# Optimization experiments

Measured on AMD Instinct MI355X. Metric: run time of the kernel, lower is better.

The kernel has to match this reference:

```python
import jax, jax.numpy as jnp
import numpy as np

B, T, D = 2, 2048, 2048
H, KV, HD = 16, 4, 128
EPS = 1e-6


def _rmsnorm(x, scale):
    # flax.linen.RMSNorm over last axis: x / sqrt(mean(x^2) + eps) * scale
    var = jnp.mean(jnp.square(x), axis=-1, keepdims=True)
    return x * jax.lax.rsqrt(var + EPS) * scale


def _rope(x, cos, sin):
    # x: [b, t, h, d]; cos/sin: [t, d]
    x_rot = jnp.stack([-x[..., 1::2], x[..., 0::2]], axis=-1)
    x_rot = x_rot.reshape(*x_rot.shape[:-2], -1)
    return x * cos[None, :, None, :] + x_rot * sin[None, :, None, :]


def setup_inputs() -> dict:
    key = jax.random.key(0)
    ks = jax.random.split(key, 5)
    x = jax.random.normal(ks[0], (B, T, D), jnp.float32)
    Wq = jax.random.normal(ks[1], (D, H * HD), jnp.float32) / np.sqrt(D)
    Wk = jax.random.normal(ks[2], (D, KV * HD), jnp.float32) / np.sqrt(D)
    Wv = jax.random.normal(ks[3], (D, KV * HD), jnp.float32) / np.sqrt(D)
    Wo = jax.random.normal(ks[4], (H * HD, D), jnp.float32) / np.sqrt(H * HD)
    q_scale = jnp.ones((HD,), jnp.float32)
    k_scale = jnp.ones((HD,), jnp.float32)
    # standard RoPE tables, interleaved-pair convention
    pos = jnp.arange(T, dtype=jnp.float32)
    inv_freq = 1.0 / (10000.0 ** (jnp.arange(0, HD, 2, dtype=jnp.float32) / HD))
    freqs = pos[:, None] * inv_freq[None, :]  # [T, HD/2]
    cos = jnp.repeat(jnp.cos(freqs), 2, axis=-1)  # [T, HD]
    sin = jnp.repeat(jnp.sin(freqs), 2, axis=-1)
    mask = jnp.tril(jnp.ones((T, T), bool))[None, None]  # causal [1,1,T,T]
    return {"x": x, "Wq": Wq, "Wk": Wk, "Wv": Wv, "Wo": Wo,
            "q_scale": q_scale, "k_scale": k_scale,
            "cos": cos, "sin": sin, "mask": mask}


def reference(x, Wq, Wk, Wv, Wo, q_scale, k_scale, cos, sin, mask):
    num_groups = H // KV
    q = (x @ Wq).reshape(B, T, H, HD)
    k = (x @ Wk).reshape(B, T, KV, HD)
    v = (x @ Wv).reshape(B, T, KV, HD)
    q = _rmsnorm(q, q_scale)
    k = _rmsnorm(k, k_scale)
    q = _rope(q, cos, sin)
    k = _rope(k, cos, sin)
    k = jnp.repeat(k, num_groups, axis=2)  # [b, t, H, d]
    v = jnp.repeat(v, num_groups, axis=2)
    scores = jnp.einsum('bqhd,bkhd->bhqk', q, k) / jnp.sqrt(jnp.float32(HD))
    scores = jnp.where(mask, scores, jnp.finfo(scores.dtype).min)
    attn = jax.nn.softmax(scores, axis=-1)
    out = jnp.einsum('bhqk,bkhd->bqhd', attn, v)
    out = out.reshape(B, T, H * HD)
    return out @ Wo
```

## Files before the change

kernel.cpp:

```cpp
#include <hip/hip_runtime.h>
#include <hip/hip_bf16.h>

#define B_   2
#define T_   2048
#define D_   2048
#define H_   16
#define KV_  4
#define HD_  128
#define BT_  (B_*T_)
#define QKVP 3072
#define KOFF 2048
#define VOFF 2560
static constexpr float EPS_ = 1e-6f;

typedef unsigned short u16;
typedef __attribute__((ext_vector_type(8))) short short8;
typedef __attribute__((ext_vector_type(4))) float f32x4;
typedef __attribute__((ext_vector_type(4))) unsigned short u16x4;

__device__ __forceinline__ u16 f2bf(float f){
    unsigned u = __float_as_uint(f);
    u += 0x7FFF + ((u >> 16) & 1);
    return (u16)(u >> 16);
}
__device__ __forceinline__ float bf2f(u16 u){
    return __uint_as_float((unsigned)u << 16);
}

__device__ __forceinline__ void async_copy16(const void* g, void* l) {
    __builtin_amdgcn_global_load_lds(
        (const __attribute__((address_space(1))) unsigned int*)g,
        (__attribute__((address_space(3))) unsigned int*)l, 16, 0, 0);
}

__global__ __launch_bounds__(256) void cvt_f32_bf16_kernel(
    const float* __restrict__ in, u16* __restrict__ out, int n)
{
    const int i = (blockIdx.x*256 + threadIdx.x)*4;
    if (i < n) {
        float4 v = *(const float4*)&in[i];
        u16x4 w = { f2bf(v.x), f2bf(v.y), f2bf(v.z), f2bf(v.w) };
        *(u16x4*)&out[i] = w;
    }
}

__global__ __launch_bounds__(256) void transpose_cvt_kernel(
    const float* __restrict__ in, u16* __restrict__ out, int R, int C)
{
    __shared__ u16 tile[64][65];
    const int r0 = blockIdx.y*64, c0 = blockIdx.x*64;
    const int tr = threadIdx.x >> 4;
    const int tc = (threadIdx.x & 15) * 4;
    #pragma unroll
    for (int i = 0; i < 4; i++) {
        const int r = tr + i*16;
        float4 v = *(const float4*)&in[(size_t)(r0 + r)*C + c0 + tc];
        tile[tc+0][r] = f2bf(v.x);
        tile[tc+1][r] = f2bf(v.y);
        tile[tc+2][r] = f2bf(v.z);
        tile[tc+3][r] = f2bf(v.w);
    }
    __syncthreads();
    #pragma unroll
    for (int i = 0; i < 4; i++) {
        const int c = tr + i*16;
        u16x4 w = { tile[c][tc+0], tile[c][tc+1], tile[c][tc+2], tile[c][tc+3] };
        *(u16x4*)&out[(size_t)(c0 + c)*R + r0 + tc] = w;
    }
}

__global__ __launch_bounds__(256) void transpose_v_kernel(
    const u16* __restrict__ qkv, u16* __restrict__ vt)
{
    __shared__ u16 tile[64][65];
    const int t0 = blockIdx.x*64;
    const int d0 = blockIdx.y*64;
    const int bk = blockIdx.z;
    const int tr = threadIdx.x >> 4;
    const int tc = (threadIdx.x & 15) * 4;
    #pragma unroll
    for (int i = 0; i < 4; i++) {
        const int t = t0 + tr + i*16;
        u16x4 v = *(const u16x4*)&qkv[(size_t)((bk>>2)*T_ + t)*QKVP + VOFF
                                      + (bk&3)*HD_ + d0 + tc];
        tile[tc+0][tr+i*16] = v[0];
        tile[tc+1][tr+i*16] = v[1];
        tile[tc+2][tr+i*16] = v[2];
        tile[tc+3][tr+i*16] = v[3];
    }
    __syncthreads();
    #pragma unroll
    for (int i = 0; i < 4; i++) {
        const int d = tr + i*16;
        u16x4 w = { tile[d][tc+0], tile[d][tc+1], tile[d][tc+2], tile[d][tc+3] };
        *(u16x4*)&vt[((size_t)bk*HD_ + d0 + d)*T_ + t0 + tc] = w;
    }
}

#define GBM 128
#define GBN 128
#define GBK 32

template<bool OUT_BF16>
__global__ __launch_bounds__(256) void gemm_mfma_kernel(
    const u16* __restrict__ A, const u16* __restrict__ Bt,
    void* __restrict__ C, int N, int K, int lda, int ldb, int ldc)
{
    __shared__ __align__(16) u16 As[GBM][GBK];
    __shared__ __align__(16) u16 Bs[GBN][GBK];
    const int tid  = threadIdx.x;
    const int lane = tid & 63;
    const int wave = tid >> 6;
    const int l15  = lane & 15;
    const int quad = lane >> 4;
    const int wr   = (wave >> 1) * 64;
    const int wc   = (wave & 1) * 64;
    const size_t row0 = (size_t)blockIdx.y * GBM;
    const size_t col0 = (size_t)blockIdx.x * GBN;

    f32x4 acc[4][4];
    #pragma unroll
    for (int i = 0; i < 4; i++)
        #pragma unroll
        for (int j = 0; j < 4; j++)
            acc[i][j] = (f32x4){0.f,0.f,0.f,0.f};

    for (int k0 = 0; k0 < K; k0 += GBK) {
        #pragma unroll
        for (int c = 0; c < 2; c++) {
            const int e = (c*256 + tid) * 8;
            const int r = e >> 5, cc = e & 31;
            async_copy16(A  + (row0 + r)*lda + k0 + cc, &As[r][cc]);
            async_copy16(Bt + (col0 + r)*ldb + k0 + cc, &Bs[r][cc]);
        }
        __syncthreads();

        short8 af[4], bf[4];
        #pragma unroll
        for (int i = 0; i < 4; i++)
            af[i] = *(const short8*)&As[wr + i*16 + l15][quad*8];
        #pragma unroll
        for (int j = 0; j < 4; j++)
            bf[j] = *(const short8*)&Bs[wc + j*16 + l15][quad*8];
        #pragma unroll
        for (int i = 0; i < 4; i++)
            #pragma unroll
            for (int j = 0; j < 4; j++)
                acc[i][j] = __builtin_amdgcn_mfma_f32_16x16x32_bf16(
                    af[i], bf[j], acc[i][j], 0, 0, 0);
        __syncthreads();
    }

    #pragma unroll
    for (int i = 0; i < 4; i++)
        #pragma unroll
        for (int r = 0; r < 4; r++) {
            const size_t row = row0 + wr + i*16 + quad*4 + r;
            #pragma unroll
            for (int j = 0; j < 4; j++) {
                const size_t col = col0 + wc + j*16 + l15;
                if (OUT_BF16) ((u16*)C)[row*ldc + col] = f2bf(acc[i][j][r]);
                else          ((float*)C)[row*ldc + col] = acc[i][j][r];
            }
        }
}

__global__ __launch_bounds__(256) void rmsnorm_rope_kernel(
    u16* __restrict__ qk, const float* __restrict__ scale,
    const float* __restrict__ cosT, const float* __restrict__ sinT,
    int heads_per_token, int head_off, float post_scale)
{
    const int wid   = blockIdx.x*4 + (threadIdx.x >> 6);
    const int lane  = threadIdx.x & 63;
    const int token = wid / heads_per_token;
    const int hidx  = wid % heads_per_token;
    const int t     = token & (T_ - 1);
    u16* p = qk + (size_t)token*QKVP + head_off + hidx*HD_ + lane*2;

    const unsigned u = *(const unsigned*)p;
    const float x0 = bf2f((u16)(u & 0xffff));
    const float x1 = bf2f((u16)(u >> 16));
    float ss = x0*x0 + x1*x1;
    #pragma unroll
    for (int off = 32; off > 0; off >>= 1) ss += __shfl_xor(ss, off);
    const float rms = rsqrtf(ss * (1.0f/HD_) + EPS_);

    const float2 sc = *(const float2*)&scale[lane*2];
    const float2 cs = *(const float2*)&cosT[(size_t)t*HD_ + lane*2];
    const float2 sn = *(const float2*)&sinT[(size_t)t*HD_ + lane*2];
    const float n0 = x0 * rms * sc.x;
    const float n1 = x1 * rms * sc.y;
    const float r0 = (n0*cs.x - n1*sn.x) * post_scale;
    const float r1 = (n1*cs.y + n0*sn.y) * post_scale;
    *(unsigned*)p = (unsigned)f2bf(r0) | ((unsigned)f2bf(r1) << 16);
}

#define BQ  64
#define BKV 64

__global__ __launch_bounds__(256, 2) void attn_mfma7_kernel(
    const u16* __restrict__ qkv, const u16* __restrict__ Vtg)
{
    __shared__ __align__(16) u16 Ks[2][16][BKV][8];
    __shared__ __align__(16) u16 Vt[2][8][HD_][8];
    __shared__ __align__(16) u16 Pb[64][88];
    __shared__ float SumX[2][64];

    const int pr   = blockIdx.x;
    const int h    = blockIdx.y;
    const int b    = blockIdx.z;
    const int kvh  = h >> 2;
    const int tid  = threadIdx.x;
    const int lane = tid & 63;
    const int wave = tid >> 6;
    const int rh   = wave >> 1;
    const int kh   = wave & 1;
    const int l15  = lane & 15;
    const int quad = lane >> 4;
    const int NT   = T_ / BQ;

    for (int phase = 0; phase < 2; phase++) {
        const int qt = phase ? pr : (NT - 1 - pr);
        const int q0 = qt * BQ;

        short8 qf[2][4];
        #pragma unroll
        for (int rf = 0; rf < 2; rf++) {
            const u16* qbase = qkv + (size_t)(b*T_ + q0 + rh*32 + rf*16 + l15)*QKVP + h*HD_;
            #pragma unroll
            for (int kt = 0; kt < 4; kt++)
                qf[rf][kt] = *(const short8*)(qbase + kt*32 + quad*8);
        }

        float lsum[2][4];
        #pragma unroll
        for (int rf = 0; rf < 2; rf++)
            #pragma unroll
            for (int r = 0; r < 4; r++) lsum[rf][r] = 0.f;
        f32x4 oacc[2][4];
        #pragma unroll
        for (int rf = 0; rf < 2; rf++)
            #pragma unroll
            for (int cv = 0; cv < 4; cv++) oacc[rf][cv] = (f32x4){0.f,0.f,0.f,0.f};

        const int ntiles = qt + 1;

        #pragma unroll
        for (int it = 0; it < 4; it++) {
            const int n   = it*256 + tid;
            const int cc  = n >> 6;
            const int key = n & 63;
            async_copy16(qkv + (size_t)(b*T_ + key)*QKVP + KOFF + kvh*HD_ + cc*8,
                         &Ks[0][cc][key][0]);
        }
        #pragma unroll
        for (int it = 0; it < 4; it++) {
            const int n  = it*256 + tid;
            const int cc = n >> 7;
            const int d  = n & 127;
            async_copy16(Vtg + ((size_t)(b*KV_ + kvh)*HD_ + d)*T_ + cc*8,
                         &Vt[0][cc][d][0]);
        }
        __syncthreads();

        int cur = 0;
        for (int t = 0; t < ntiles; t++) {
            if (t + 1 < ntiles) {
                const int k0n = (t + 1) * BKV;
                #pragma unroll
                for (int it = 0; it < 4; it++) {
                    const int n   = it*256 + tid;
                    const int cc  = n >> 6;
                    const int key = n & 63;
                    async_copy16(qkv + (size_t)(b*T_ + k0n + key)*QKVP + KOFF + kvh*HD_ + cc*8,
                                 &Ks[cur^1][cc][key][0]);
                }
                #pragma unroll
                for (int it = 0; it < 4; it++) {
                    const int n  = it*256 + tid;
                    const int cc = n >> 7;
                    const int d  = n & 127;
                    async_copy16(Vtg + ((size_t)(b*KV_ + kvh)*HD_ + d)*T_ + k0n + cc*8,
                                 &Vt[cur^1][cc][d][0]);
                }
            }

            const int k0 = t * BKV;

            f32x4 s[2][2];
            #pragma unroll
            for (int rf = 0; rf < 2; rf++)
                #pragma unroll
                for (int cj = 0; cj < 2; cj++) s[rf][cj] = (f32x4){0.f,0.f,0.f,0.f};
            __builtin_amdgcn_s_setprio(1);
            #pragma unroll
            for (int kt = 0; kt < 4; kt++) {
                #pragma unroll
                for (int cj = 0; cj < 2; cj++) {
                    short8 kf = *(const short8*)&Ks[cur][kt*4 + quad][kh*32 + cj*16 + l15][0];
                    #pragma unroll
                    for (int rf = 0; rf < 2; rf++)
                        s[rf][cj] = __builtin_amdgcn_mfma_f32_16x16x32_bf16(
                            qf[rf][kt], kf, s[rf][cj], 0, 0, 0);
                }
            }
            __builtin_amdgcn_s_setprio(0);

            if (t == ntiles - 1) {
                #pragma unroll
                for (int rf = 0; rf < 2; rf++) {
                    const int qrow0 = q0 + rh*32 + rf*16 + quad*4;
                    #pragma unroll
                    for (int r = 0; r < 4; r++)
                        #pragma unroll
                        for (int cj = 0; cj < 2; cj++) {
                            const int key = k0 + kh*32 + cj*16 + l15;
                            if (key > qrow0 + r) s[rf][cj][r] = -1e30f;
                        }
                }
            }
            #pragma unroll
            for (int rf = 0; rf < 2; rf++)
                #pragma unroll
                for (int r = 0; r < 4; r++)
                    #pragma unroll
                    for (int cj = 0; cj < 2; cj++) {
                        const float p = __expf(s[rf][cj][r]);
                        s[rf][cj][r] = p;
                        lsum[rf][r] += p;
                        Pb[rh*32 + rf*16 + quad*4 + r][kh*32 + cj*16 + l15] = f2bf(p);
                    }

            asm volatile("s_waitcnt lgkmcnt(0)" ::: "memory");
            __builtin_amdgcn_s_barrier();

            __builtin_amdgcn_s_setprio(1);
            #pragma unroll
            for (int kt2 = 0; kt2 < 2; kt2++) {
                short8 pa[2];
                #pragma unroll
                for (int rf = 0; rf < 2; rf++)
                    pa[rf] = *(const short8*)&Pb[rh*32 + rf*16 + l15][kt2*32 + quad*8];
                #pragma unroll
                for (int cv = 0; cv < 4; cv++) {
                    short8 vf = *(const short8*)&Vt[cur][kt2*4 + quad][kh*64 + cv*16 + l15][0];
                    #pragma unroll
                    for (int rf = 0; rf < 2; rf++)
                        oacc[rf][cv] = __builtin_amdgcn_mfma_f32_16x16x32_bf16(
                            pa[rf], vf, oacc[rf][cv], 0, 0, 0);
                }
            }
            __builtin_amdgcn_s_setprio(0);

            __syncthreads();
            cur ^= 1;
        }

        #pragma unroll
        for (int rf = 0; rf < 2; rf++)
            #pragma unroll
            for (int r = 0; r < 4; r++) {
                float tot = lsum[rf][r];
                #pragma unroll
                for (int off = 1; off < 16; off <<= 1)
                    tot += __shfl_xor(tot, off, 16);
                if (l15 == 0) SumX[kh][rh*32 + rf*16 + quad*4 + r] = tot;
            }
        __syncthreads();
        #pragma unroll
        for (int rf = 0; rf < 2; rf++)
            #pragma unroll
            for (int r = 0; r < 4; r++) {
                const int rIdx = rh*32 + rf*16 + quad*4 + r;
                const float linv = 1.0f / (SumX[0][rIdx] + SumX[1][rIdx]);
                u16* orow = (u16*)qkv + (size_t)(b*T_ + q0 + rIdx)*QKVP
                            + h*HD_ + kh*64 + l15;
                #pragma unroll
                for (int cv = 0; cv < 4; cv++)
                    orow[cv*16] = f2bf(oacc[rf][cv][r] * linv);
            }
        __syncthreads();
    }
}

extern "C" void kernel_launch(void* const* d_in, const int* in_sizes, int n_in,
                              void* d_out, int out_size, void* d_ws, size_t ws_size,
                              hipStream_t stream)
{
    const float* x    = (const float*)d_in[0];
    const float* Wq   = (const float*)d_in[1];
    const float* Wk   = (const float*)d_in[2];
    const float* Wv   = (const float*)d_in[3];
    const float* Wo   = (const float*)d_in[4];
    const float* qsc  = (const float*)d_in[5];
    const float* ksc  = (const float*)d_in[6];
    const float* cosT = (const float*)d_in[7];
    const float* sinT = (const float*)d_in[8];
    float* out = (float*)d_out;

    u16* xb     = (u16*)d_ws;
    u16* Wqkvt  = xb    + (size_t)BT_*D_;
    u16* Wot    = Wqkvt + (size_t)QKVP*D_;
    u16* qkv    = Wot   + (size_t)D_*(H_*HD_);
    u16* vtg    = qkv   + (size_t)BT_*QKVP;

    cvt_f32_bf16_kernel<<<(BT_*D_)/1024, 256, 0, stream>>>(x, xb, BT_*D_);
    transpose_cvt_kernel<<<dim3((H_*HD_)/64,  D_/64), 256, 0, stream>>>(
        Wq, Wqkvt, D_, H_*HD_);
    transpose_cvt_kernel<<<dim3((KV_*HD_)/64, D_/64), 256, 0, stream>>>(
        Wk, Wqkvt + (size_t)KOFF*D_, D_, KV_*HD_);
    transpose_cvt_kernel<<<dim3((KV_*HD_)/64, D_/64), 256, 0, stream>>>(
        Wv, Wqkvt + (size_t)VOFF*D_, D_, KV_*HD_);
    transpose_cvt_kernel<<<dim3(D_/64, (H_*HD_)/64),  256, 0, stream>>>(
        Wo, Wot, H_*HD_, D_);

    gemm_mfma_kernel<true><<<dim3(QKVP/GBN, BT_/GBM), 256, 0, stream>>>(
        xb, Wqkvt, qkv, QKVP, D_, D_, D_, QKVP);

    rmsnorm_rope_kernel<<<(BT_*H_)/4,  256, 0, stream>>>(
        qkv, qsc, cosT, sinT, H_, 0, 0.08838834764831845f);
    rmsnorm_rope_kernel<<<(BT_*KV_)/4, 256, 0, stream>>>(
        qkv, ksc, cosT, sinT, KV_, KOFF, 1.0f);

    transpose_v_kernel<<<dim3(T_/64, HD_/64, B_*KV_), 256, 0, stream>>>(qkv, vtg);

    attn_mfma7_kernel<<<dim3(T_/BQ/2, H_, B_), 256, 0, stream>>>(qkv, vtg);

    gemm_mfma_kernel<false><<<dim3(D_/GBN, BT_/GBM), 256, 0, stream>>>(
        qkv, Wot, out, D_, D_, QKVP, D_, D_);
}
```

Before: 379.1 us.

## Enlarge attention query tile to 128 with per-wave full-key rows

The attention kernel now handles 128 query rows per block, with each wave owning 32 rows across the full 64-key tile and the full 128-wide head dimension. This removes the cross-wave split of keys, so the mid-tile barrier, the shared-memory sum exchange and the two-phase loop are dropped, and P is staged in per-wave LDS. Load balancing changes from pairing a heavy and a light tile inside one block to reversing tile order by batch index. The cost is more accumulator registers (oacc doubles) and fewer blocks in flight, since the grid stays the same size while each block covers more queries.

Result: no change. 380.1 us (+0.2%).

```diff
diff --git a/kernel.cpp b/kernel.cpp
--- a/kernel.cpp
+++ b/kernel.cpp
@@ -195,192 +195,171 @@
     *(unsigned*)p = (unsigned)f2bf(r0) | ((unsigned)f2bf(r1) << 16);
 }
 
-#define BQ  64
+#define BQ2 128
 #define BKV 64
 
-__global__ __launch_bounds__(256, 2) void attn_mfma7_kernel(
+__global__ __launch_bounds__(256, 2) void attn_mfma12_kernel(
     const u16* __restrict__ qkv, const u16* __restrict__ Vtg)
 {
     __shared__ __align__(16) u16 Ks[2][16][BKV][8];
     __shared__ __align__(16) u16 Vt[2][8][HD_][8];
-    __shared__ __align__(16) u16 Pb[64][88];
-    __shared__ float SumX[2][64];
-
-    const int pr   = blockIdx.x;
+    __shared__ __align__(16) u16 Pb[4][2][8][16][8];
+
+    const int x    = blockIdx.x;
     const int h    = blockIdx.y;
     const int b    = blockIdx.z;
+    const int qt   = b ? x : 15 - x;
     const int kvh  = h >> 2;
     const int tid  = threadIdx.x;
     const int lane = tid & 63;
     const int wave = tid >> 6;
-    const int rh   = wave >> 1;
-    const int kh   = wave & 1;
     const int l15  = lane & 15;
     const int quad = lane >> 4;
-    const int NT   = T_ / BQ;
-
-    for (int phase = 0; phase < 2; phase++) {
-        const int qt = phase ? pr : (NT - 1 - pr);
-        const int q0 = qt * BQ;
-
-        short8 qf[2][4];
-        #pragma unroll
-        for (int rf = 0; rf < 2; rf++) {
-            const u16* qbase = qkv + (size_t)(b*T_ + q0 + rh*32 + rf*16 + l15)*QKVP + h*HD_;
-            #pragma unroll
-            for (int kt = 0; kt < 4; kt++)
-                qf[rf][kt] = *(const short8*)(qbase + kt*32 + quad*8);
-        }
-
-        float lsum[2][4];
+    const int q0   = qt * BQ2;
+    const int ntiles = 2*qt + 2;
+
+    short8 qf[2][4];
+    #pragma unroll
+    for (int rf = 0; rf < 2; rf++) {
+        const u16* qbase = qkv + (size_t)(b*T_ + q0 + rf*64 + wave*16 + l15)*QKVP + h*HD_;
+        #pragma unroll
+        for (int kt = 0; kt < 4; kt++)
+            qf[rf][kt] = *(const short8*)(qbase + kt*32 + quad*8);
+    }
+
+    float lsum[2][4];
+    #pragma unroll
+    for (int rf = 0; rf < 2; rf++)
+        #pragma unroll
+        for (int r = 0; r < 4; r++) lsum[rf][r] = 0.f;
+    f32x4 oacc[2][8];
+    #pragma unroll
+    for (int rf = 0; rf < 2; rf++)
+        #pragma unroll
+        for (int cv = 0; cv < 8; cv++) oacc[rf][cv] = (f32x4){0.f,0.f,0.f,0.f};
+
+    #pragma unroll
+    for (int it = 0; it < 4; it++) {
+        const int n2  = it*256 + tid;
+        const int cc  = n2 >> 6;
+        const int key = n2 & 63;
+        async_copy16(qkv + (size_t)(b*T_ + key)*QKVP + KOFF + kvh*HD_ + cc*8,
+                     &Ks[0][cc][key][0]);
+    }
+    #pragma unroll
+    for (int it = 0; it < 4; it++) {
+        const int n2 = it*256 + tid;
+        const int cc = n2 >> 7;
+        const int d  = n2 & 127;
+        async_copy16(Vtg + ((size_t)(b*KV_ + kvh)*HD_ + d)*T_ + cc*8,
+                     &Vt[0][cc][d][0]);
+    }
+    __syncthreads();
+
+    int cur = 0;
+    for (int t = 0; t < ntiles; t++) {
+        if (t + 1 < ntiles) {
+            const int k0n = (t + 1) * BKV;
+            #pragma unroll
+            for (int it = 0; it < 4; it++) {
+                const int n2  = it*256 + tid;
+                const int cc  = n2 >> 6;
+                const int key = n2 & 63;
+                async_copy16(qkv + (size_t)(b*T_ + k0n + key)*QKVP + KOFF + kvh*HD_ + cc*8,
+                             &Ks[cur^1][cc][key][0]);
+            }
+            #pragma unroll
+            for (int it = 0; it < 4; it++) {
+                const int n2 = it*256 + tid;
+                const int cc = n2 >> 7;
+                const int d  = n2 & 127;
+                async_copy16(Vtg + ((size_t)(b*KV_ + kvh)*HD_ + d)*T_ + k0n + cc*8,
+                             &Vt[cur^1][cc][d][0]);
+            }
+        }
+
+        const int k0 = t * BKV;
+
+        f32x4 s[2][4];
         #pragma unroll
         for (int rf = 0; rf < 2; rf++)
             #pragma unroll
-            for (int r = 0; r < 4; r++) lsum[rf][r] = 0.f;
-        f32x4 oacc[2][4];
-        #pragma unroll
-        for (int rf = 0; rf < 2; rf++)
-            #pragma unroll
-            for (int cv = 0; cv < 4; cv++) oacc[rf][cv] = (f32x4){0.f,0.f,0.f,0.f};
-
-        const int ntiles = qt + 1;
-
-        #pragma unroll
-        for (int it = 0; it < 4; it++) {
-            const int n   = it*256 + tid;
-            const int cc  = n >> 6;
-            const int key = n & 63;
-            async_copy16(qkv + (size_t)(b*T_ + key)*QKVP + KOFF + kvh*HD_ + cc*8,
-                         &Ks[0][cc][key][0]);
-        }
-        #pragma unroll
-        for (int it = 0; it < 4; it++) {
-            const int n  = it*256 + tid;
-            const int cc = n >> 7;
-            const int d  = n & 127;
-            async_copy16(Vtg + ((size_t)(b*KV_ + kvh)*HD_ + d)*T_ + cc*8,
-                         &Vt[0][cc][d][0]);
-        }
-        __syncthreads();
-
-        int cur = 0;
-        for (int t = 0; t < ntiles; t++) {
-            if (t + 1 < ntiles) {
-                const int k0n = (t + 1) * BKV;
+            for (int c = 0; c < 4; c++) s[rf][c] = (f32x4){0.f,0.f,0.f,0.f};
+        __builtin_amdgcn_s_setprio(1);
+        #pragma unroll
+        for (int kt = 0; kt < 4; kt++) {
+            #pragma unroll
+            for (int c = 0; c < 4; c++) {
+                short8 kf = *(const short8*)&Ks[cur][kt*4 + quad][c*16 + l15][0];
                 #pragma unroll
-                for (int it = 0; it < 4; it++) {
-                    const int n   = it*256 + tid;
-                    const int cc  = n >> 6;
-                    const int key = n & 63;
-                    async_copy16(qkv + (size_t)(b*T_ + k0n + key)*QKVP + KOFF + kvh*HD_ + cc*8,
-                                 &Ks[cur^1][cc][key][0]);
-                }
-                #pragma unroll
-                for (int it = 0; it < 4; it++) {
-                    const int n  = it*256 + tid;
-                    const int cc = n >> 7;
-                    const int d  = n & 127;
-                    async_copy16(Vtg + ((size_t)(b*KV_ + kvh)*HD_ + d)*T_ + k0n + cc*8,
-                                 &Vt[cur^1][cc][d][0]);
-                }
-            }
-
-            const int k0 = t * BKV;
-
-            f32x4 s[2][2];
-            #pragma unroll
-            for (int rf = 0; rf < 2; rf++)
-                #pragma unroll
-                for (int cj = 0; cj < 2; cj++) s[rf][cj] = (f32x4){0.f,0.f,0.f,0.f};
-            __builtin_amdgcn_s_setprio(1);
-            #pragma unroll
-            for (int kt = 0; kt < 4; kt++) {
-                #pragma unroll
-                for (int cj = 0; cj < 2; cj++) {
-                    short8 kf = *(const short8*)&Ks[cur][kt*4 + quad][kh*32 + cj*16 + l15][0];
-                    #pragma unroll
-                    for (int rf = 0; rf < 2; rf++)
-                        s[rf][cj] = __builtin_amdgcn_mfma_f32_16x16x32_bf16(
-                            qf[rf][kt], kf, s[rf][cj], 0, 0, 0);
-                }
-            }
-            __builtin_amdgcn_s_setprio(0);
-
-            if (t == ntiles - 1) {
-                #pragma unroll
-                for (int rf = 0; rf < 2; rf++) {
-                    const int qrow0 = q0 + rh*32 + rf*16 + quad*4;
-                    #pragma unroll
-                    for (int r = 0; r < 4; r++)
-                        #pragma unroll
-                        for (int cj = 0; cj < 2; cj++) {
-                            const int key = k0 + kh*32 + cj*16 + l15;
-                            if (key > qrow0 + r) s[rf][cj][r] = -1e30f;
-                        }
-                }
-            }
-            #pragma unroll
-            for (int rf = 0; rf < 2; rf++)
+                for (int rf = 0; rf < 2; rf++)
+                    s[rf][c] = __builtin_amdgcn_mfma_f32_16x16x32_bf16(
+                        qf[rf][kt], kf, s[rf][c], 0, 0, 0);
+            }
+        }
+        __builtin_amdgcn_s_setprio(0);
+
+        if (t >= ntiles - 2) {
+            #pragma unroll
+            for (int rf = 0; rf < 2; rf++) {
+                const int qrow0 = q0 + rf*64 + wave*16 + quad*4;
                 #pragma unroll
                 for (int r = 0; r < 4; r++)
                     #pragma unroll
-                    for (int cj = 0; cj < 2; cj++) {
-                        const float p = __expf(s[rf][cj][r]);
-                        s[rf][cj][r] = p;
-                        lsum[rf][r] += p;
-                        Pb[rh*32 + rf*16 + quad*4 + r][kh*32 + cj*16 + l15] = f2bf(p);
+                    for (int c = 0; c < 4; c++) {
+                        const int key = k0 + c*16 + l15;
+                        if (key > qrow0 + r) s[rf][c][r] = -1e30f;
                     }
-
-            asm volatile("s_waitcnt lgkmcnt(0)" ::: "memory");
-            __builtin_amdgcn_s_barrier();
-
-            __builtin_amdgcn_s_setprio(1);
-            #pragma unroll
-            for (int kt2 = 0; kt2 < 2; kt2++) {
-                short8 pa[2];
+            }
+        }
+        #pragma unroll
+        for (int rf = 0; rf < 2; rf++)
+            #pragma unroll
+            for (int r = 0; r < 4; r++)
+                #pragma unroll
+                for (int c = 0; c < 4; c++) {
+                    const float p = __expf(s[rf][c][r]);
+                    lsum[rf][r] += p;
+                    Pb[wave][rf][c*2 + (l15 >> 3)][quad*4 + r][l15 & 7] = f2bf(p);
+                }
+
+        __builtin_amdgcn_s_setprio(1);
+        #pragma unroll
+        for (int kt2 = 0; kt2 < 2; kt2++) {
+            short8 pa[2];
+            #pragma unroll
+            for (int rf = 0; rf < 2; rf++)
+                pa[rf] = *(const short8*)&Pb[wave][rf][kt2*4 + quad][l15][0];
+            #pragma unroll
+            for (int cv = 0; cv < 8; cv++) {
+                short8 vf = *(const short8*)&Vt[cur][kt2*4 + quad][cv*16 + l15][0];
                 #pragma unroll
                 for (int rf = 0; rf < 2; rf++)
-                    pa[rf] = *(const short8*)&Pb[rh*32 + rf*16 + l15][kt2*32 + quad*8];
-                #pragma unroll
-                for (int cv = 0; cv < 4; cv++) {
-                    short8 vf = *(const short8*)&Vt[cur][kt2*4 + quad][kh*64 + cv*16 + l15][0];
-                    #pragma unroll
-                    for (int rf = 0; rf < 2; rf++)
-                        oacc[rf][cv] = __builtin_amdgcn_mfma_f32_16x16x32_bf16(
-                            pa[rf], vf, oacc[rf][cv], 0, 0, 0);
-                }
-            }
-            __builtin_amdgcn_s_setprio(0);
-
-            __syncthreads();
-            cur ^= 1;
-        }
-
-        #pragma unroll
-        for (int rf = 0; rf < 2; rf++)
-            #pragma unroll
-            for (int r = 0; r < 4; r++) {
-                float tot = lsum[rf][r];
-                #pragma unroll
-                for (int off = 1; off < 16; off <<= 1)
-                    tot += __shfl_xor(tot, off, 16);
-                if (l15 == 0) SumX[kh][rh*32 + rf*16 + quad*4 + r] = tot;
-            }
+                    oacc[rf][cv] = __builtin_amdgcn_mfma_f32_16x16x32_bf16(
+                        pa[rf], vf, oacc[rf][cv], 0, 0, 0);
+            }
+        }
+        __builtin_amdgcn_s_setprio(0);
+
         __syncthreads();
-        #pragma unroll
-        for (int rf = 0; rf < 2; rf++)
-            #pragma unroll
-            for (int r = 0; r < 4; r++) {
-                const int rIdx = rh*32 + rf*16 + quad*4 + r;
-                const float linv = 1.0f / (SumX[0][rIdx] + SumX[1][rIdx]);
-                u16* orow = (u16*)qkv + (size_t)(b*T_ + q0 + rIdx)*QKVP
-                            + h*HD_ + kh*64 + l15;
-                #pragma unroll
-                for (int cv = 0; cv < 4; cv++)
-                    orow[cv*16] = f2bf(oacc[rf][cv][r] * linv);
-            }
-        __syncthreads();
-    }
+        cur ^= 1;
+    }
+
+    #pragma unroll
+    for (int rf = 0; rf < 2; rf++)
+        #pragma unroll
+        for (int r = 0; r < 4; r++) {
+            float tot = lsum[rf][r];
+            #pragma unroll
+            for (int off = 1; off < 16; off <<= 1)
+                tot += __shfl_xor(tot, off, 16);
+            const float linv = 1.0f / tot;
+            u16* orow = (u16*)qkv + (size_t)(b*T_ + q0 + rf*64 + wave*16 + quad*4 + r)*QKVP
+                        + h*HD_ + l15;
+            #pragma unroll
+            for (int cv = 0; cv < 8; cv++)
+                orow[cv*16] = f2bf(oacc[rf][cv][r] * linv);
+        }
 }
 
 extern "C" void kernel_launch(void* const* d_in, const int* in_sizes, int n_in,
@@ -424,7 +403,7 @@
 
     transpose_v_kernel<<<dim3(T_/64, HD_/64, B_*KV_), 256, 0, stream>>>(qkv, vtg);
 
-    attn_mfma7_kernel<<<dim3(T_/BQ/2, H_, B_), 256, 0, stream>>>(qkv, vtg);
+    attn_mfma12_kernel<<<dim3(T_/BQ2, H_, B_), 256, 0, stream>>>(qkv, vtg);
 
     gemm_mfma_kernel<false><<<dim3(D_/GBN, BT_/GBM), 256, 0, stream>>>(
         qkv, Wot, out, D_, D_, QKVP, D_, D_);
```
